# Performance work log

Measured on AMD Instinct MI355X. Metric: run time of the kernel, lower is better.

The kernel has to match this reference:

```python
import jax, jax.numpy as jnp
import numpy as np

IN_FEATURES = 4096
OUT_FEATURES = 4096
BLOCKSIZE = 64
FP4_CODEBOOK = np.array([0.0, 0.0052, 0.6667, 1.0, 0.3333, 0.5, 0.1667, 0.25,
                         0.0, -0.0052, -0.6667, -1.0, -0.3333, -0.5, -0.1667, -0.25],
                        dtype=np.float32)


def setup_inputs() -> dict:
    key = jax.random.key(0)
    k1, k2, k3, k4 = jax.random.split(key, 4)
    n_elements = OUT_FEATURES * IN_FEATURES
    n_blocks = n_elements // BLOCKSIZE
    x = jax.random.normal(k1, (4, 2048, IN_FEATURES), dtype=jnp.float32)
    weight_packed = jax.random.randint(k2, (n_elements // 2,), 0, 256, dtype=jnp.int32)
    scale = jax.random.uniform(k3, (n_blocks,), dtype=jnp.float32)
    bias = jax.random.normal(k4, (OUT_FEATURES,), dtype=jnp.float32)
    return {"x": x, "weight_packed": weight_packed, "scale": scale, "bias": bias}


def reference(x, weight_packed, scale, bias):
    codebook = jnp.asarray(FP4_CODEBOOK, dtype=x.dtype)
    # Unpack two 4-bit indices per byte: high nibble first, then low nibble.
    high = (weight_packed >> 4) & 15
    low = weight_packed & 15
    indices = jnp.stack([high, low], axis=1).reshape(-1)  # [n_elements]
    # LUT dequant + per-block scale broadcast.
    deq = codebook[indices].reshape(-1, BLOCKSIZE) * scale[:, None]  # [n_blocks, blocksize]
    weight = deq.reshape(OUT_FEATURES, IN_FEATURES)
    # F.linear(x, W, b) = x @ W.T + b
    return jnp.einsum('bsi,oi->bso', x, weight) + bias
```

## Files before the change

### kernel.cpp

```cpp
#include <hip/hip_runtime.h>
#include <stdint.h>
#include <stddef.h>

#define IN_F 4096
#define OUT_F 4096
#define M_TOT 8192
#define BM 128
#define BN 128
#define BK 64

typedef __attribute__((ext_vector_type(8))) short short8;
typedef __attribute__((ext_vector_type(4))) float f32x4;
typedef __attribute__((ext_vector_type(4))) float float4v;
typedef __attribute__((ext_vector_type(4))) unsigned short u16x4;
typedef __attribute__((ext_vector_type(8))) unsigned short u16x8;
typedef unsigned short u16;

__constant__ float c_lut[16] = {
  0.0f, 0.0052f, 0.6667f, 1.0f, 0.3333f, 0.5f, 0.1667f, 0.25f,
  0.0f, -0.0052f, -0.6667f, -1.0f, -0.3333f, -0.5f, -0.1667f, -0.25f
};

__device__ __forceinline__ u16 f2bf(float f) {
  unsigned int x = __float_as_uint(f);
  x += 0x7fffu + ((x >> 16) & 1u);
  return (u16)(x >> 16);
}

__device__ __forceinline__ void gload_lds16(const u16* g, u16* lds) {
  __builtin_amdgcn_global_load_lds(
      (const __attribute__((address_space(1))) unsigned int*)g,
      (__attribute__((address_space(3))) unsigned int*)lds, 16, 0, 0);
}

__global__ __launch_bounds__(256) void k_convert_x(const float* __restrict__ x,
                                                   u16* __restrict__ a) {
  const int n8 = (M_TOT * IN_F) / 8;
  const int stride = gridDim.x * blockDim.x;
  for (int t = blockIdx.x * blockDim.x + threadIdx.x; t < n8; t += stride) {
    float4v f0 = ((const float4v*)x)[2 * t];
    float4v f1 = ((const float4v*)x)[2 * t + 1];
    u16x8 o;
    o[0] = f2bf(f0.x); o[1] = f2bf(f0.y); o[2] = f2bf(f0.z); o[3] = f2bf(f0.w);
    o[4] = f2bf(f1.x); o[5] = f2bf(f1.y); o[6] = f2bf(f1.z); o[7] = f2bf(f1.w);
    ((u16x8*)a)[t] = o;
  }
}

__global__ __launch_bounds__(256) void k_dequant_w(const int* __restrict__ wp,
                                                   const float* __restrict__ scale,
                                                   u16* __restrict__ b) {
  __shared__ float lut[16];
  if (threadIdx.x < 16) lut[threadIdx.x] = c_lut[threadIdx.x];
  __syncthreads();
  const int ng = (OUT_F * IN_F / 2) / 4;
  const int stride = gridDim.x * blockDim.x;
  for (int t = blockIdx.x * blockDim.x + threadIdx.x; t < ng; t += stride) {
    int4 p = ((const int4*)wp)[t];
    float s = scale[t >> 3];
    int by[4] = {p.x, p.y, p.z, p.w};
    u16x8 o;
#pragma unroll
    for (int q = 0; q < 4; ++q) {
      o[2 * q]     = f2bf(lut[(by[q] >> 4) & 15] * s);
      o[2 * q + 1] = f2bf(lut[by[q] & 15] * s);
    }
    ((u16x8*)b)[t] = o;
  }
}

__global__ __launch_bounds__(256) void k_gemm(const u16* __restrict__ A,
                                              const u16* __restrict__ B,
                                              const float* __restrict__ bias,
                                              float* __restrict__ C) {
  __shared__ u16 As[BM * BK];
  __shared__ u16 Bs[BN * BK];
  const int tid  = threadIdx.x;
  const int lane = tid & 63;
  const int wave = tid >> 6;
  const int mBase = blockIdx.y * BM;
  const int nBase = blockIdx.x * BN;
  const int wm = (wave >> 1) * 64;
  const int wn = (wave & 1) * 64;

  const int srow = lane >> 3;
  const int scol = ((lane & 7) ^ srow) * 8;

  const int frow = lane & 15;
  const int fx   = lane & 7;
  const int cq   = lane >> 4;

  f32x4 acc[4][4] = {};

  for (int kt = 0; kt < IN_F; kt += BK) {
#pragma unroll
    for (int i = 0; i < 4; ++i) {
      const int r0 = wave * 32 + i * 8;
      gload_lds16(A + (size_t)(mBase + r0 + srow) * IN_F + kt + scol, &As[r0 * BK]);
      gload_lds16(B + (size_t)(nBase + r0 + srow) * IN_F + kt + scol, &Bs[r0 * BK]);
    }
    asm volatile("s_waitcnt vmcnt(0)" ::: "memory");
    __syncthreads();

#pragma unroll
    for (int ks = 0; ks < BK; ks += 32) {
      const int co = (((ks >> 3) + cq) ^ fx) << 3;
      short8 a[4], b[4];
#pragma unroll
      for (int i = 0; i < 4; ++i)
        a[i] = *(const short8*)&As[(wm + i * 16 + frow) * BK + co];
#pragma unroll
      for (int j = 0; j < 4; ++j)
        b[j] = *(const short8*)&Bs[(wn + j * 16 + frow) * BK + co];
#pragma unroll
      for (int i = 0; i < 4; ++i)
#pragma unroll
        for (int j = 0; j < 4; ++j)
          acc[i][j] = __builtin_amdgcn_mfma_f32_16x16x32_bf16(a[i], b[j], acc[i][j], 0, 0, 0);
    }
    __syncthreads();
  }

  const int ccol = lane & 15;
  const int crow = (lane >> 4) * 4;
#pragma unroll
  for (int j = 0; j < 4; ++j) {
    const int col = nBase + wn + j * 16 + ccol;
    const float bv = bias[col];
#pragma unroll
    for (int i = 0; i < 4; ++i) {
      const size_t rb = (size_t)(mBase + wm + i * 16 + crow) * OUT_F + col;
#pragma unroll
      for (int t = 0; t < 4; ++t)
        C[rb + (size_t)t * OUT_F] = acc[i][j][t] + bv;
    }
  }
}

__global__ __launch_bounds__(256) void k_gemm_fused(const float* __restrict__ X,
                                                    const int* __restrict__ WP,
                                                    const float* __restrict__ scale,
                                                    const float* __restrict__ bias,
                                                    float* __restrict__ C) {
  __shared__ u16 As[BM * BK];
  __shared__ u16 Bs[BN * BK];
  __shared__ float lut[16];
  const int tid = threadIdx.x;
  if (tid < 16) lut[tid] = c_lut[tid];
  const int lane = tid & 63;
  const int wave = tid >> 6;
  const int mBase = blockIdx.y * BM;
  const int nBase = blockIdx.x * BN;
  const int wm = (wave >> 1) * 64;
  const int wn = (wave & 1) * 64;
  const int frow = lane & 15;
  const int fx   = lane & 7;
  const int cq   = lane >> 4;
  f32x4 acc[4][4] = {};
  __syncthreads();

  for (int kt = 0; kt < IN_F; kt += BK) {
#pragma unroll
    for (int i = 0; i < 8; ++i) {
      const int g = tid + i * 256;
      const int r = g >> 4, c = (g & 15) * 4;
      float4v f = *(const float4v*)&X[(size_t)(mBase + r) * IN_F + kt + c];
      u16x4 o;
      o.x = f2bf(f.x); o.y = f2bf(f.y); o.z = f2bf(f.z); o.w = f2bf(f.w);
      *(u16x4*)&As[r * BK + ((((c >> 3) ^ (r & 7)) << 3) | (c & 7))] = o;
    }
#pragma unroll
    for (int i = 0; i < 4; ++i) {
      const int g = tid + i * 256;
      const int r = g >> 3, c4 = (g & 7) * 4;
      int4 p = *(const int4*)&WP[(size_t)(nBase + r) * (IN_F / 2) + (kt >> 1) + c4];
      const float s = scale[(nBase + r) * 64 + (kt >> 6)];
      int by[4] = {p.x, p.y, p.z, p.w};
      u16x8 o;
#pragma unroll
      for (int q = 0; q < 4; ++q) {
        o[2 * q]     = f2bf(lut[(by[q] >> 4) & 15] * s);
        o[2 * q + 1] = f2bf(lut[by[q] & 15] * s);
      }
      *(u16x8*)&Bs[r * BK + (((g & 7) ^ (r & 7)) << 3)] = o;
    }
    __syncthreads();
#pragma unroll
    for (int ks = 0; ks < BK; ks += 32) {
      const int co = (((ks >> 3) + cq) ^ fx) << 3;
      short8 a[4], b[4];
#pragma unroll
      for (int i = 0; i < 4; ++i)
        a[i] = *(const short8*)&As[(wm + i * 16 + frow) * BK + co];
#pragma unroll
      for (int j = 0; j < 4; ++j)
        b[j] = *(const short8*)&Bs[(wn + j * 16 + frow) * BK + co];
#pragma unroll
      for (int i = 0; i < 4; ++i)
#pragma unroll
        for (int j = 0; j < 4; ++j)
          acc[i][j] = __builtin_amdgcn_mfma_f32_16x16x32_bf16(a[i], b[j], acc[i][j], 0, 0, 0);
    }
    __syncthreads();
  }

  const int ccol = lane & 15;
  const int crow = (lane >> 4) * 4;
#pragma unroll
  for (int j = 0; j < 4; ++j) {
    const int col = nBase + wn + j * 16 + ccol;
    const float bv = bias[col];
#pragma unroll
    for (int i = 0; i < 4; ++i) {
      const size_t rb = (size_t)(mBase + wm + i * 16 + crow) * OUT_F + col;
#pragma unroll
      for (int t = 0; t < 4; ++t)
        C[rb + (size_t)t * OUT_F] = acc[i][j][t] + bv;
    }
  }
}

extern "C" void kernel_launch(void* const* d_in, const int* in_sizes, int n_in,
                              void* d_out, int out_size, void* d_ws, size_t ws_size,
                              hipStream_t stream) {
  const float* x  = (const float*)d_in[0];
  const int*   wp = (const int*)d_in[1];
  const float* sc = (const float*)d_in[2];
  const float* bi = (const float*)d_in[3];
  float* out = (float*)d_out;

  const size_t bBytes = (size_t)OUT_F * IN_F * 2;
  const size_t aBytes = (size_t)M_TOT * IN_F * 2;
  dim3 grid(OUT_F / BN, M_TOT / BM);

  if (ws_size >= aBytes + bBytes) {
    u16* B = (u16*)d_ws;
    u16* A = (u16*)((char*)d_ws + bBytes);
    k_dequant_w<<<2048, 256, 0, stream>>>(wp, sc, B);
    k_convert_x<<<4096, 256, 0, stream>>>(x, A);
    k_gemm<<<grid, 256, 0, stream>>>(A, B, bi, out);
  } else {
    k_gemm_fused<<<grid, 256, 0, stream>>>(x, wp, sc, bi, out);
  }
}
```

Before: 548.0 us.

## Replace bf16 GEMM with 256x256 double-buffered 8-wave pipelined kernel

Replaces the 128x128 single-buffered GEMM with a 256x256-tile, 512-thread kernel that double-buffers A/B in LDS and interleaves half-tile global->LDS loads with four MFMA quadrants per K step, using partial vmcnt waits, barriers and s_setprio. It also remaps block IDs so tiles sharing rows/columns land on the same XCD for L2 reuse. The larger tile raises arithmetic intensity and the pipelining hides load latency behind MFMA work. The cost is more registers (8x4 accumulators per wave), 128KB of LDS per block, and a fragile hand-tuned wait/barrier schedule.

```diff
diff --git a/kernel.cpp b/kernel.cpp
--- a/kernel.cpp
+++ b/kernel.cpp
@@ -5,9 +5,15 @@
 #define IN_F 4096
 #define OUT_F 4096
 #define M_TOT 8192
+
 #define BM 128
 #define BN 128
 #define BK 64
+
+#define BM2 256
+#define BN2 256
+#define BK2 64
+#define NT2 (IN_F / BK2)
 
 typedef __attribute__((ext_vector_type(8))) short short8;
 typedef __attribute__((ext_vector_type(4))) float f32x4;
@@ -32,6 +38,11 @@
       (const __attribute__((address_space(1))) unsigned int*)g,
       (__attribute__((address_space(3))) unsigned int*)lds, 16, 0, 0);
 }
+
+#define BARRIER() do { asm volatile("" ::: "memory"); \
+                       __builtin_amdgcn_s_barrier();  \
+                       asm volatile("" ::: "memory"); } while (0)
+#define LGKM0() asm volatile("s_waitcnt lgkmcnt(0)" ::: "memory")
 
 __global__ __launch_bounds__(256) void k_convert_x(const float* __restrict__ x,
                                                    u16* __restrict__ a) {
@@ -69,56 +80,154 @@
   }
 }
 
-__global__ __launch_bounds__(256) void k_gemm(const u16* __restrict__ A,
-                                              const u16* __restrict__ B,
-                                              const float* __restrict__ bias,
-                                              float* __restrict__ C) {
-  __shared__ u16 As[BM * BK];
-  __shared__ u16 Bs[BN * BK];
+
+__device__ __forceinline__ void stage_a_half(const u16* __restrict__ A, u16* dst,
+                                             int mBase, int kt, int h,
+                                             int wave, int srow, int scol) {
+#pragma unroll
+  for (int n = 0; n < 2; ++n) {
+    const int r0 = n * 128 + h * 64 + wave * 8;
+    gload_lds16(A + (size_t)(mBase + r0 + srow) * IN_F + kt + scol, dst + r0 * BK2);
+  }
+}
+
+__device__ __forceinline__ void stage_b_half(const u16* __restrict__ B, u16* dst,
+                                             int nBase, int kt, int jh,
+                                             int wave, int srow, int scol) {
+#pragma unroll
+  for (int n = 0; n < 2; ++n) {
+    const int slot = wave * 2 + n;
+    const int r0 = (slot >> 2) * 64 + jh * 32 + (slot & 3) * 8;
+    gload_lds16(B + (size_t)(nBase + r0 + srow) * IN_F + kt + scol, dst + r0 * BK2);
+  }
+}
+
+__device__ __forceinline__ void read_a4(const u16* As_c, int aBase, int co0, int co1,
+                                        short8 a[4][2], int h) {
+#pragma unroll
+  for (int ii = 0; ii < 4; ++ii) {
+    const int ro = aBase + (h * 4 + ii) * (16 * BK2);
+    a[ii][0] = *(const short8*)&As_c[ro + co0];
+    a[ii][1] = *(const short8*)&As_c[ro + co1];
+  }
+}
+
+__device__ __forceinline__ void read_b2(const u16* Bs_c, int bBase, int co0, int co1,
+                                        short8 b[2][2], int jh) {
+#pragma unroll
+  for (int jj = 0; jj < 2; ++jj) {
+    const int ro = bBase + (jh * 2 + jj) * (16 * BK2);
+    b[jj][0] = *(const short8*)&Bs_c[ro + co0];
+    b[jj][1] = *(const short8*)&Bs_c[ro + co1];
+  }
+}
+
+__device__ __forceinline__ void mma_quad(f32x4 acc[8][4], const short8 a[4][2],
+                                         const short8 b[2][2], int h, int jh) {
+#pragma unroll
+  for (int k2 = 0; k2 < 2; ++k2)
+#pragma unroll
+    for (int ii = 0; ii < 4; ++ii)
+#pragma unroll
+      for (int jj = 0; jj < 2; ++jj)
+        acc[h * 4 + ii][jh * 2 + jj] = __builtin_amdgcn_mfma_f32_16x16x32_bf16(
+            a[ii][k2], b[jj][k2], acc[h * 4 + ii][jh * 2 + jj], 0, 0, 0);
+}
+
+__global__ __launch_bounds__(512, 2) void k_gemm256(const u16* __restrict__ A,
+                                                    const u16* __restrict__ B,
+                                                    const float* __restrict__ bias,
+                                                    float* __restrict__ C) {
+  __shared__ u16 As[2][BM2 * BK2];
+  __shared__ u16 Bs[2][BN2 * BK2];
+
   const int tid  = threadIdx.x;
   const int lane = tid & 63;
   const int wave = tid >> 6;
-  const int mBase = blockIdx.y * BM;
-  const int nBase = blockIdx.x * BN;
-  const int wm = (wave >> 1) * 64;
-  const int wn = (wave & 1) * 64;
+
+  const int bid   = blockIdx.x;
+  const int xcd   = bid & 7;
+  const int k     = bid >> 3;
+  const int tileM = (xcd >> 1) * 8 + (k >> 3);
+  const int tileN = (xcd & 1) * 8 + (k & 7);
+  const int mBase = tileM * BM2;
+  const int nBase = tileN * BN2;
+
+  const int wm = (wave >> 2) * 128;
+  const int wn = (wave & 3) * 64;
 
   const int srow = lane >> 3;
   const int scol = ((lane & 7) ^ srow) * 8;
 
   const int frow = lane & 15;
-  const int fx   = lane & 7;
+  const int fx   = frow & 7;
   const int cq   = lane >> 4;
-
-  f32x4 acc[4][4] = {};
-
-  for (int kt = 0; kt < IN_F; kt += BK) {
-#pragma unroll
-    for (int i = 0; i < 4; ++i) {
-      const int r0 = wave * 32 + i * 8;
-      gload_lds16(A + (size_t)(mBase + r0 + srow) * IN_F + kt + scol, &As[r0 * BK]);
-      gload_lds16(B + (size_t)(nBase + r0 + srow) * IN_F + kt + scol, &Bs[r0 * BK]);
-    }
-    asm volatile("s_waitcnt vmcnt(0)" ::: "memory");
-    __syncthreads();
-
-#pragma unroll
-    for (int ks = 0; ks < BK; ks += 32) {
-      const int co = (((ks >> 3) + cq) ^ fx) << 3;
-      short8 a[4], b[4];
-#pragma unroll
-      for (int i = 0; i < 4; ++i)
-        a[i] = *(const short8*)&As[(wm + i * 16 + frow) * BK + co];
-#pragma unroll
-      for (int j = 0; j < 4; ++j)
-        b[j] = *(const short8*)&Bs[(wn + j * 16 + frow) * BK + co];
-#pragma unroll
-      for (int i = 0; i < 4; ++i)
-#pragma unroll
-        for (int j = 0; j < 4; ++j)
-          acc[i][j] = __builtin_amdgcn_mfma_f32_16x16x32_bf16(a[i], b[j], acc[i][j], 0, 0, 0);
-    }
-    __syncthreads();
+  const int co0  = ((cq ^ fx) << 3);
+  const int co1  = (((4 + cq) ^ fx) << 3);
+  const int aBase = (wm + frow) * BK2;
+  const int bBase = (wn + frow) * BK2;
+
+  f32x4 acc[8][4] = {};
+
+  stage_a_half(A, As[0], mBase, 0, 0, wave, srow, scol);
+  stage_a_half(A, As[0], mBase, 0, 1, wave, srow, scol);
+  stage_b_half(B, Bs[0], nBase, 0, 0, wave, srow, scol);
+  stage_b_half(B, Bs[0], nBase, 0, 1, wave, srow, scol);
+  stage_a_half(A, As[1], mBase, BK2, 0, wave, srow, scol);
+  stage_b_half(B, Bs[1], nBase, BK2, 1, wave, srow, scol);
+  stage_a_half(A, As[1], mBase, BK2, 1, wave, srow, scol);
+  asm volatile("s_waitcnt vmcnt(6)" ::: "memory");
+  BARRIER();
+
+  short8 a[4][2], b[2][2];
+
+#pragma unroll 2
+  for (int t = 0; t < NT2; ++t) {
+    const int c = t & 1;
+    u16* AsC = As[c];
+    u16* BsC = Bs[c];
+    u16* BsO = Bs[c ^ 1];
+    const int kt1 = (t + 1) * BK2;
+    const int kt2 = (t + 2) * BK2;
+
+    read_a4(AsC, aBase, co0, co1, a, 0);
+    read_b2(BsC, bBase, co0, co1, b, 0);
+    if (t + 1 < NT2) stage_b_half(B, BsO, nBase, kt1, 0, wave, srow, scol);
+    BARRIER();
+    LGKM0();
+    __builtin_amdgcn_s_setprio(1);
+    mma_quad(acc, a, b, 0, 0);
+    __builtin_amdgcn_s_setprio(0);
+    BARRIER();
+
+    read_b2(BsC, bBase, co0, co1, b, 1);
+    if (t + 2 < NT2) stage_a_half(A, AsC, mBase, kt2, 0, wave, srow, scol);
+    BARRIER();
+    LGKM0();
+    __builtin_amdgcn_s_setprio(1);
+    mma_quad(acc, a, b, 0, 1);
+    __builtin_amdgcn_s_setprio(0);
+    BARRIER();
+
+    read_a4(AsC, aBase, co0, co1, a, 1);
+    if (t + 2 < NT2) stage_b_half(B, BsC, nBase, kt2, 1, wave, srow, scol);
+    BARRIER();
+    LGKM0();
+    __builtin_amdgcn_s_setprio(1);
+    mma_quad(acc, a, b, 1, 1);
+    __builtin_amdgcn_s_setprio(0);
+    BARRIER();
+
+    read_b2(BsC, bBase, co0, co1, b, 0);
+    if (t + 2 < NT2) stage_a_half(A, AsC, mBase, kt2, 1, wave, srow, scol);
+    BARRIER();
+    LGKM0();
+    __builtin_amdgcn_s_setprio(1);
+    mma_quad(acc, a, b, 1, 0);
+    __builtin_amdgcn_s_setprio(0);
+    if (t < NT2 - 2) asm volatile("s_waitcnt vmcnt(6)" ::: "memory");
+    else             asm volatile("s_waitcnt vmcnt(0)" ::: "memory");
+    BARRIER();
   }
 
   const int ccol = lane & 15;
@@ -128,11 +237,11 @@
     const int col = nBase + wn + j * 16 + ccol;
     const float bv = bias[col];
 #pragma unroll
-    for (int i = 0; i < 4; ++i) {
+    for (int i = 0; i < 8; ++i) {
       const size_t rb = (size_t)(mBase + wm + i * 16 + crow) * OUT_F + col;
 #pragma unroll
-      for (int t = 0; t < 4; ++t)
-        C[rb + (size_t)t * OUT_F] = acc[i][j][t] + bv;
+      for (int tt = 0; tt < 4; ++tt)
+        C[rb + (size_t)tt * OUT_F] = acc[i][j][tt] + bv;
     }
   }
 }
@@ -231,15 +340,15 @@
 
   const size_t bBytes = (size_t)OUT_F * IN_F * 2;
   const size_t aBytes = (size_t)M_TOT * IN_F * 2;
-  dim3 grid(OUT_F / BN, M_TOT / BM);
 
   if (ws_size >= aBytes + bBytes) {
     u16* B = (u16*)d_ws;
     u16* A = (u16*)((char*)d_ws + bBytes);
     k_dequant_w<<<2048, 256, 0, stream>>>(wp, sc, B);
     k_convert_x<<<4096, 256, 0, stream>>>(x, A);
-    k_gemm<<<grid, 256, 0, stream>>>(A, B, bi, out);
+    k_gemm256<<<(M_TOT / BM2) * (OUT_F / BN2), 512, 0, stream>>>(A, B, bi, out);
   } else {
+    dim3 grid(OUT_F / BN, M_TOT / BM);
     k_gemm_fused<<<grid, 256, 0, stream>>>(x, wp, sc, bi, out);
   }
 }
```

New measurement: 489.0 us. 1.12x faster.
